# Optimization experiments

Hardware: AMD Instinct MI355X
Metric: run time of the kernel (lower is better)

Reference implementation:

```python
import jax, jax.numpy as jnp
import numpy as np

B, P, D, H = 4, 2048, 768, 12
DFF = 4 * D
EPS = 1e-3  # Keras LayerNormalization default epsilon
SURVIVAL_PROB = 0.9  # inference-mode droppath scaling


def setup_inputs() -> dict:
    key = jax.random.key(0)
    ks = jax.random.split(key, 4)
    s = 0.02
    return {
        "x": jax.random.normal(ks[0], (B, P, D), dtype=jnp.float32),
        "ln1_g": jnp.ones((D,), jnp.float32),
        "ln1_b": jnp.zeros((D,), jnp.float32),
        "w_qkv": jax.random.normal(ks[1], (D, 3 * D), jnp.float32) * s,
        "b_qkv": jnp.zeros((3 * D,), jnp.float32),
        "ln2_g": jnp.ones((D,), jnp.float32),
        "ln2_b": jnp.zeros((D,), jnp.float32),
        "w1": jax.random.normal(ks[2], (D, DFF), jnp.float32) * s,
        "b1": jnp.zeros((DFF,), jnp.float32),
        "w2": jax.random.normal(ks[3], (DFF, D), jnp.float32) * s,
        "b2": jnp.zeros((D,), jnp.float32),
    }


def _layernorm(x, g, b):
    mu = jnp.mean(x, axis=-1, keepdims=True)
    var = jnp.mean(jnp.square(x - mu), axis=-1, keepdims=True)
    return (x - mu) * jax.lax.rsqrt(var + EPS) * g + b


def _block(x, ln1_g, ln1_b, w_qkv, b_qkv, ln2_g, ln2_b, w1, b1, w2, b2):
    # --- pre-norm self-attention ---
    h = _layernorm(x, ln1_g, ln1_b)
    qkv = h @ w_qkv + b_qkv                      # [B,P,3D]
    q, k, v = jnp.split(qkv, 3, axis=-1)
    hd = D // H
    to_heads = lambda t: t.reshape(B, P, H, hd).transpose(0, 2, 1, 3)  # b h p c
    q, k, v = to_heads(q), to_heads(k), to_heads(v)
    scale = jnp.sqrt(jnp.float32(D / H))
    scores = jnp.einsum('bhqc,bhkc->bhqk', q, k) / scale
    attn = jax.nn.softmax(scores, axis=-1)
    o = jnp.einsum('bhqk,bhkc->bhqc', attn, v)
    o = o.transpose(0, 2, 1, 3).reshape(B, P, D)
    x = o * SURVIVAL_PROB + x
    # --- pre-norm MLP ---
    h = _layernorm(x, ln2_g, ln2_b)
    h = jax.nn.gelu(h @ w1 + b1, approximate=False)
    h = h @ w2 + b2
    return h * SURVIVAL_PROB + x


def reference(x, ln1_g, ln1_b, w_qkv, b_qkv, ln2_g, ln2_b, w1, b1, w2, b2):
    return _block(x, ln1_g, ln1_b, w_qkv, b_qkv, ln2_g, ln2_b, w1, b1, w2, b2)
```

## Files before the change

kernel.cpp:

```cpp
#include <hip/hip_runtime.h>
#include <hip/hip_bf16.h>
#include <math.h>

#define B_ 4
#define P_ 2048
#define D_ 768
#define H_ 12

typedef __attribute__((ext_vector_type(8))) short bf16x8;
typedef __attribute__((ext_vector_type(4))) float f32x4;

static __device__ __forceinline__ short f2bf(float f) {
  union { float f; unsigned u; } z; z.f = f;
  unsigned r = z.u + 0x7fffu + ((z.u >> 16) & 1u);
  return (short)(r >> 16);
}

static __device__ __forceinline__ void gll16(const void* g, void* l) {
  __builtin_amdgcn_global_load_lds(
      (const __attribute__((address_space(1))) void*)g,
      (__attribute__((address_space(3))) void*)l, 16, 0, 0);
}

static __device__ __forceinline__ int vswz(int d) {
  return ((d & 7) ^ ((d >> 3) & 7)) << 3;
}

__global__ __launch_bounds__(256) void tcvt_kernel(const float* __restrict__ in,
                                                   short* __restrict__ out, int K, int N) {
  __shared__ float t[32][33];
  int k0 = blockIdx.x * 32, n0 = blockIdx.y * 32;
  int tx = threadIdx.x & 31, ty = threadIdx.x >> 5;
#pragma unroll
  for (int i = 0; i < 4; ++i)
    t[ty + 8 * i][tx] = in[(size_t)(k0 + ty + 8 * i) * N + n0 + tx];
  __syncthreads();
#pragma unroll
  for (int i = 0; i < 4; ++i)
    out[(size_t)(n0 + ty + 8 * i) * K + k0 + tx] = f2bf(t[tx][ty + 8 * i]);
}

__global__ __launch_bounds__(256) void ln_kernel(const float* __restrict__ in,
                                                 const float* __restrict__ g,
                                                 const float* __restrict__ be,
                                                 short* __restrict__ out) {
  int row = blockIdx.x, tid = threadIdx.x;
  const float* xr = in + (size_t)row * D_;
  float v0 = xr[tid], v1 = xr[tid + 256], v2 = xr[tid + 512];
  float s = v0 + v1 + v2;
  float ss = v0 * v0 + v1 * v1 + v2 * v2;
#pragma unroll
  for (int d = 1; d < 64; d <<= 1) {
    s += __shfl_xor(s, d, 64);
    ss += __shfl_xor(ss, d, 64);
  }
  __shared__ float red[8];
  int w = tid >> 6;
  if ((tid & 63) == 0) { red[w] = s; red[4 + w] = ss; }
  __syncthreads();
  s = red[0] + red[1] + red[2] + red[3];
  ss = red[4] + red[5] + red[6] + red[7];
  float mu = s * (1.0f / D_);
  float rstd = rsqrtf(ss * (1.0f / D_) - mu * mu + 1e-3f);
  short* orow = out + (size_t)row * D_;
  orow[tid]       = f2bf((v0 - mu) * rstd * g[tid]       + be[tid]);
  orow[tid + 256] = f2bf((v1 - mu) * rstd * g[tid + 256] + be[tid + 256]);
  orow[tid + 512] = f2bf((v2 - mu) * rstd * g[tid + 512] + be[tid + 512]);
}

template <int EPI>
__global__ __launch_bounds__(256, 3) void gemm128(
    const short* __restrict__ A, const short* __restrict__ Bt,
    const float* __restrict__ bias, short* __restrict__ out_bf,
    float* __restrict__ out_f, const float* __restrict__ resid,
    int M, int N, int K) {
  alignas(16) __shared__ short a_lds[128 * 32];
  alignas(16) __shared__ short b_lds[128 * 32];
  const int tid = threadIdx.x;
  const int wv = tid >> 6, lane = tid & 63;
  const int wm = wv >> 1, wn = wv & 1;
  const int g = lane >> 4, r = lane & 15;
  const int m0 = blockIdx.x * 128, n0 = blockIdx.y * 128;
  const int srow = lane >> 2, sseg = lane & 3;
  f32x4 acc[4][4] = {};
  const short* aptr = A + (size_t)(m0 + wv * 16 + srow) * K + sseg * 8;
  const short* bptr = Bt + (size_t)(n0 + wv * 16 + srow) * K + sseg * 8;
  short* alds0 = &a_lds[(wv * 16) * 32];
  short* blds0 = &b_lds[(wv * 16) * 32];
  for (int k0 = 0; k0 < K; k0 += 32) {
    __syncthreads();
    gll16(aptr + k0, alds0);
    gll16(aptr + k0 + (size_t)64 * K, alds0 + 64 * 32);
    gll16(bptr + k0, blds0);
    gll16(bptr + k0 + (size_t)64 * K, blds0 + 64 * 32);
    __syncthreads();
    bf16x8 af[4], bfr[4];
#pragma unroll
    for (int i = 0; i < 4; ++i)
      af[i] = *reinterpret_cast<const bf16x8*>(&a_lds[(wm * 64 + i * 16 + r) * 32 + g * 8]);
#pragma unroll
    for (int i = 0; i < 4; ++i)
      bfr[i] = *reinterpret_cast<const bf16x8*>(&b_lds[(wn * 64 + i * 16 + r) * 32 + g * 8]);
#pragma unroll
    for (int i = 0; i < 4; ++i)
#pragma unroll
      for (int jn = 0; jn < 4; ++jn)
        acc[i][jn] = __builtin_amdgcn_mfma_f32_16x16x32_bf16(af[i], bfr[jn], acc[i][jn], 0, 0, 0);
  }
#pragma unroll
  for (int i = 0; i < 4; ++i) {
#pragma unroll
    for (int jn = 0; jn < 4; ++jn) {
      int col = n0 + wn * 64 + jn * 16 + r;
      float bb = bias[col];
#pragma unroll
      for (int jj = 0; jj < 4; ++jj) {
        int row = m0 + wm * 64 + i * 16 + g * 4 + jj;
        float v = acc[i][jn][jj] + bb;
        size_t idx = (size_t)row * N + col;
        if (EPI == 0) {
          out_bf[idx] = f2bf(v);
        } else if (EPI == 1) {
          v = 0.5f * v * (1.0f + erff(v * 0.70710678118654752f));
          out_bf[idx] = f2bf(v);
        } else {
          out_f[idx] = v * 0.9f + resid[idx];
        }
      }
    }
  }
}

__global__ __launch_bounds__(256, 3) void attn_kernel(const short* __restrict__ qkv,
                                                      const float* __restrict__ x,
                                                      float* __restrict__ x2) {
  alignas(16) __shared__ short k_lds[64 * 72];
  alignas(16) __shared__ short vt_lds[64 * 64];
  alignas(16) __shared__ short p_lds[4][32 * 72];
  const int tid = threadIdx.x, wv = tid >> 6, lane = tid & 63;
  const int g = lane >> 4, r = lane & 15;
  const int b = blockIdx.y / H_, h = blockIdx.y % H_;
  const int TD = 3 * D_;
  const int qrow0 = blockIdx.x * 128 + wv * 32;
  bf16x8 qf[2][2];
#pragma unroll
  for (int mf = 0; mf < 2; ++mf)
#pragma unroll
    for (int kb = 0; kb < 2; ++kb)
      qf[mf][kb] = *reinterpret_cast<const bf16x8*>(
          qkv + (size_t)(b * P_ + qrow0 + mf * 16 + r) * TD + h * 64 + kb * 32 + g * 8);
  f32x4 acc[2][4] = {};
  float m_run[2][4], l_run[2][4];
#pragma unroll
  for (int mf = 0; mf < 2; ++mf)
#pragma unroll
    for (int j = 0; j < 4; ++j) { m_run[mf][j] = -1e30f; l_run[mf][j] = 0.0f; }
  const int lrow = tid >> 2, lseg = tid & 3;
  short* p_w = &p_lds[wv][0];
  for (int kc = 0; kc < P_; kc += 64) {
    const short* src = qkv + (size_t)(b * P_ + kc + lrow) * TD + D_ + h * 64 + lseg * 16;
    bf16x8 kv0 = *reinterpret_cast<const bf16x8*>(src);
    bf16x8 kv1 = *reinterpret_cast<const bf16x8*>(src + 8);
    bf16x8 vv0 = *reinterpret_cast<const bf16x8*>(src + D_);
    bf16x8 vv1 = *reinterpret_cast<const bf16x8*>(src + D_ + 8);
    __syncthreads();
    *reinterpret_cast<bf16x8*>(&k_lds[lrow * 72 + lseg * 16]) = kv0;
    *reinterpret_cast<bf16x8*>(&k_lds[lrow * 72 + lseg * 16 + 8]) = kv1;
#pragma unroll
    for (int j = 0; j < 8; ++j) {
      int d0 = lseg * 16 + j, d1 = d0 + 8;
      vt_lds[d0 * 64 + (lrow ^ vswz(d0))] = vv0[j];
      vt_lds[d1 * 64 + (lrow ^ vswz(d1))] = vv1[j];
    }
    __syncthreads();
    f32x4 sc[2][4];
#pragma unroll
    for (int cf = 0; cf < 4; ++cf) {
      bf16x8 kf0 = *reinterpret_cast<const bf16x8*>(&k_lds[(cf * 16 + r) * 72 + g * 8]);
      bf16x8 kf1 = *reinterpret_cast<const bf16x8*>(&k_lds[(cf * 16 + r) * 72 + 32 + g * 8]);
#pragma unroll
      for (int mf = 0; mf < 2; ++mf) {
        f32x4 s = {};
        s = __builtin_amdgcn_mfma_f32_16x16x32_bf16(qf[mf][0], kf0, s, 0, 0, 0);
        s = __builtin_amdgcn_mfma_f32_16x16x32_bf16(qf[mf][1], kf1, s, 0, 0, 0);
        sc[mf][cf] = s;
      }
    }
#pragma unroll
    for (int mf = 0; mf < 2; ++mf) {
#pragma unroll
      for (int j = 0; j < 4; ++j) {
        float s0 = sc[mf][0][j] * 0.125f, s1 = sc[mf][1][j] * 0.125f;
        float s2 = sc[mf][2][j] * 0.125f, s3 = sc[mf][3][j] * 0.125f;
        float mt = fmaxf(fmaxf(s0, s1), fmaxf(s2, s3));
#pragma unroll
        for (int d = 1; d < 16; d <<= 1) mt = fmaxf(mt, __shfl_xor(mt, d, 64));
        float mn = fmaxf(m_run[mf][j], mt);
        float corr = __expf(m_run[mf][j] - mn);
        m_run[mf][j] = mn;
        float p0 = __expf(s0 - mn), p1 = __expf(s1 - mn);
        float p2 = __expf(s2 - mn), p3 = __expf(s3 - mn);
        float ls = p0 + p1 + p2 + p3;
#pragma unroll
        for (int d = 1; d < 16; d <<= 1) ls += __shfl_xor(ls, d, 64);
        l_run[mf][j] = l_run[mf][j] * corr + ls;
#pragma unroll
        for (int cf = 0; cf < 4; ++cf) acc[mf][cf][j] *= corr;
        int prow = (mf * 16 + g * 4 + j) * 72;
        p_w[prow + 0 + r]  = f2bf(p0);
        p_w[prow + 16 + r] = f2bf(p1);
        p_w[prow + 32 + r] = f2bf(p2);
        p_w[prow + 48 + r] = f2bf(p3);
      }
    }
    bf16x8 vf[4][2];
#pragma unroll
    for (int cf = 0; cf < 4; ++cf) {
      int d = cf * 16 + r;
      int sw = vswz(d);
      vf[cf][0] = *reinterpret_cast<const bf16x8*>(&vt_lds[d * 64 + ((g * 8) ^ sw)]);
      vf[cf][1] = *reinterpret_cast<const bf16x8*>(&vt_lds[d * 64 + ((32 + g * 8) ^ sw)]);
    }
#pragma unroll
    for (int mf = 0; mf < 2; ++mf) {
      bf16x8 pf0 = *reinterpret_cast<const bf16x8*>(&p_w[(mf * 16 + r) * 72 + g * 8]);
      bf16x8 pf1 = *reinterpret_cast<const bf16x8*>(&p_w[(mf * 16 + r) * 72 + 32 + g * 8]);
#pragma unroll
      for (int cf = 0; cf < 4; ++cf) {
        acc[mf][cf] = __builtin_amdgcn_mfma_f32_16x16x32_bf16(pf0, vf[cf][0], acc[mf][cf], 0, 0, 0);
        acc[mf][cf] = __builtin_amdgcn_mfma_f32_16x16x32_bf16(pf1, vf[cf][1], acc[mf][cf], 0, 0, 0);
      }
    }
  }
#pragma unroll
  for (int mf = 0; mf < 2; ++mf)
#pragma unroll
    for (int cf = 0; cf < 4; ++cf) {
      int col = h * 64 + cf * 16 + r;
#pragma unroll
      for (int j = 0; j < 4; ++j) {
        int row = qrow0 + mf * 16 + g * 4 + j;
        size_t idx = (size_t)(b * P_ + row) * D_ + col;
        x2[idx] = (acc[mf][cf][j] / l_run[mf][j]) * 0.9f + x[idx];
      }
    }
}

extern "C" void kernel_launch(void* const* d_in, const int* in_sizes, int n_in,
                              void* d_out, int out_size, void* d_ws, size_t ws_size,
                              hipStream_t stream) {
  const float* x     = (const float*)d_in[0];
  const float* ln1_g = (const float*)d_in[1];
  const float* ln1_b = (const float*)d_in[2];
  const float* w_qkv = (const float*)d_in[3];
  const float* b_qkv = (const float*)d_in[4];
  const float* ln2_g = (const float*)d_in[5];
  const float* ln2_b = (const float*)d_in[6];
  const float* w1    = (const float*)d_in[7];
  const float* b1    = (const float*)d_in[8];
  const float* w2    = (const float*)d_in[9];
  const float* b2    = (const float*)d_in[10];
  float* out = (float*)d_out;
  char* ws = (char*)d_ws;

  short* wqkv_t = (short*)(ws);
  short* w1_t   = (short*)(ws + 3538944);
  short* w2_t   = (short*)(ws + 8257536);
  short* h_bf   = (short*)(ws + 12976128);
  short* qkv_bf = (short*)(ws + 25559040);
  short* a1_bf  = qkv_bf;

  const int R = B_ * P_;

  { dim3 g2(768 / 32, 2304 / 32);  tcvt_kernel<<<g2, 256, 0, stream>>>(w_qkv, wqkv_t, 768, 2304); }
  { dim3 g2(768 / 32, 3072 / 32);  tcvt_kernel<<<g2, 256, 0, stream>>>(w1, w1_t, 768, 3072); }
  { dim3 g2(3072 / 32, 768 / 32);  tcvt_kernel<<<g2, 256, 0, stream>>>(w2, w2_t, 3072, 768); }

  ln_kernel<<<R, 256, 0, stream>>>(x, ln1_g, ln1_b, h_bf);

  {
    dim3 grid(R / 128, 2304 / 128);
    gemm128<0><<<grid, 256, 0, stream>>>(h_bf, wqkv_t, b_qkv, qkv_bf, nullptr, nullptr,
                                         R, 2304, 768);
  }
  {
    dim3 grid(P_ / 128, B_ * H_);
    attn_kernel<<<grid, 256, 0, stream>>>(qkv_bf, x, out);
  }
  ln_kernel<<<R, 256, 0, stream>>>(out, ln2_g, ln2_b, h_bf);
  {
    dim3 grid(R / 128, 3072 / 128);
    gemm128<1><<<grid, 256, 0, stream>>>(h_bf, w1_t, b1, a1_bf, nullptr, nullptr,
                                         R, 3072, 768);
  }
  {
    dim3 grid(R / 128, 768 / 128);
    gemm128<2><<<grid, 256, 0, stream>>>(a1_bf, w2_t, b2, nullptr, out, out,
                                         R, 768, 3072);
  }
}
```

Before: 460.7 us.

## Compute transposed attention scores so softmax reductions stay mostly in-lane

Swaps the MFMA operands so each lane holds scores for one query row across several keys. The row max and sum then need only two cross-lane shuffles instead of four per row-slot, and P is written to LDS with packed bf16 stores. The 1/8 scale is folded into Q once, with bf16 rounding, and the final normalisation uses a reciprocal broadcast by shuffle. The per-row correction factor now needs extra shuffles to reach the accumulator layout, and pre-scaling Q in bf16 slightly changes rounding.

```diff
diff --git a/kernel.cpp b/kernel.cpp
--- a/kernel.cpp
+++ b/kernel.cpp
@@ -14,6 +14,12 @@
   union { float f; unsigned u; } z; z.f = f;
   unsigned r = z.u + 0x7fffu + ((z.u >> 16) & 1u);
   return (short)(r >> 16);
+}
+
+static __device__ __forceinline__ float bf2f(short s) {
+  union { unsigned u; float f; } z;
+  z.u = ((unsigned)(unsigned short)s) << 16;
+  return z.f;
 }
 
 static __device__ __forceinline__ void gll16(const void* g, void* l) {
@@ -146,17 +152,20 @@
 #pragma unroll
   for (int mf = 0; mf < 2; ++mf)
 #pragma unroll
-    for (int kb = 0; kb < 2; ++kb)
-      qf[mf][kb] = *reinterpret_cast<const bf16x8*>(
+    for (int kb = 0; kb < 2; ++kb) {
+      bf16x8 q = *reinterpret_cast<const bf16x8*>(
           qkv + (size_t)(b * P_ + qrow0 + mf * 16 + r) * TD + h * 64 + kb * 32 + g * 8);
+#pragma unroll
+      for (int e = 0; e < 8; ++e) q[e] = f2bf(bf2f(q[e]) * 0.125f);
+      qf[mf][kb] = q;
+    }
   f32x4 acc[2][4] = {};
-  float m_run[2][4], l_run[2][4];
-#pragma unroll
-  for (int mf = 0; mf < 2; ++mf)
-#pragma unroll
-    for (int j = 0; j < 4; ++j) { m_run[mf][j] = -1e30f; l_run[mf][j] = 0.0f; }
+  float m_run[2], l_run[2];
+#pragma unroll
+  for (int mf = 0; mf < 2; ++mf) { m_run[mf] = -1e30f; l_run[mf] = 0.0f; }
   const int lrow = tid >> 2, lseg = tid & 3;
   short* p_w = &p_lds[wv][0];
+  const int bcast = 20 * g;
   for (int kc = 0; kc < P_; kc += 64) {
     const short* src = qkv + (size_t)(b * P_ + kc + lrow) * TD + D_ + h * 64 + lseg * 16;
     bf16x8 kv0 = *reinterpret_cast<const bf16x8*>(src);
@@ -173,7 +182,7 @@
       vt_lds[d1 * 64 + (lrow ^ vswz(d1))] = vv1[j];
     }
     __syncthreads();
-    f32x4 sc[2][4];
+    f32x4 st[2][4];
 #pragma unroll
     for (int cf = 0; cf < 4; ++cf) {
       bf16x8 kf0 = *reinterpret_cast<const bf16x8*>(&k_lds[(cf * 16 + r) * 72 + g * 8]);
@@ -181,36 +190,53 @@
 #pragma unroll
       for (int mf = 0; mf < 2; ++mf) {
         f32x4 s = {};
-        s = __builtin_amdgcn_mfma_f32_16x16x32_bf16(qf[mf][0], kf0, s, 0, 0, 0);
-        s = __builtin_amdgcn_mfma_f32_16x16x32_bf16(qf[mf][1], kf1, s, 0, 0, 0);
-        sc[mf][cf] = s;
+        s = __builtin_amdgcn_mfma_f32_16x16x32_bf16(kf0, qf[mf][0], s, 0, 0, 0);
+        s = __builtin_amdgcn_mfma_f32_16x16x32_bf16(kf1, qf[mf][1], s, 0, 0, 0);
+        st[mf][cf] = s;
       }
     }
 #pragma unroll
     for (int mf = 0; mf < 2; ++mf) {
-#pragma unroll
-      for (int j = 0; j < 4; ++j) {
-        float s0 = sc[mf][0][j] * 0.125f, s1 = sc[mf][1][j] * 0.125f;
-        float s2 = sc[mf][2][j] * 0.125f, s3 = sc[mf][3][j] * 0.125f;
-        float mt = fmaxf(fmaxf(s0, s1), fmaxf(s2, s3));
-#pragma unroll
-        for (int d = 1; d < 16; d <<= 1) mt = fmaxf(mt, __shfl_xor(mt, d, 64));
-        float mn = fmaxf(m_run[mf][j], mt);
-        float corr = __expf(m_run[mf][j] - mn);
-        m_run[mf][j] = mn;
-        float p0 = __expf(s0 - mn), p1 = __expf(s1 - mn);
-        float p2 = __expf(s2 - mn), p3 = __expf(s3 - mn);
-        float ls = p0 + p1 + p2 + p3;
-#pragma unroll
-        for (int d = 1; d < 16; d <<= 1) ls += __shfl_xor(ls, d, 64);
-        l_run[mf][j] = l_run[mf][j] * corr + ls;
-#pragma unroll
-        for (int cf = 0; cf < 4; ++cf) acc[mf][cf][j] *= corr;
-        int prow = (mf * 16 + g * 4 + j) * 72;
-        p_w[prow + 0 + r]  = f2bf(p0);
-        p_w[prow + 16 + r] = f2bf(p1);
-        p_w[prow + 32 + r] = f2bf(p2);
-        p_w[prow + 48 + r] = f2bf(p3);
+      float mx = st[mf][0][0];
+#pragma unroll
+      for (int cf = 0; cf < 4; ++cf)
+#pragma unroll
+        for (int j = 0; j < 4; ++j) mx = fmaxf(mx, st[mf][cf][j]);
+      mx = fmaxf(mx, __shfl_xor(mx, 16, 64));
+      mx = fmaxf(mx, __shfl_xor(mx, 32, 64));
+      float mn = fmaxf(m_run[mf], mx);
+      float corr = __expf(m_run[mf] - mn);
+      m_run[mf] = mn;
+      float p[4][4];
+      float ls = 0.0f;
+#pragma unroll
+      for (int cf = 0; cf < 4; ++cf)
+#pragma unroll
+        for (int j = 0; j < 4; ++j) {
+          float pv = __expf(st[mf][cf][j] - mn);
+          p[cf][j] = pv;
+          ls += pv;
+        }
+      ls += __shfl_xor(ls, 16, 64);
+      ls += __shfl_xor(ls, 32, 64);
+      l_run[mf] = l_run[mf] * corr + ls;
+      short* prow = &p_w[(mf * 16 + r) * 72];
+#pragma unroll
+      for (int cf = 0; cf < 4; ++cf) {
+        __hip_bfloat162 lo = __float22bfloat162_rn(make_float2(p[cf][0], p[cf][1]));
+        __hip_bfloat162 hi = __float22bfloat162_rn(make_float2(p[cf][2], p[cf][3]));
+        union { __hip_bfloat162 h2; unsigned u; } c0, c1;
+        c0.h2 = lo; c1.h2 = hi;
+        *reinterpret_cast<uint2*>(&prow[cf * 16 + 4 * g]) = make_uint2(c0.u, c1.u);
+      }
+      float cb0 = __shfl(corr, bcast + 0, 64);
+      float cb1 = __shfl(corr, bcast + 1, 64);
+      float cb2 = __shfl(corr, bcast + 2, 64);
+      float cb3 = __shfl(corr, bcast + 3, 64);
+#pragma unroll
+      for (int cf = 0; cf < 4; ++cf) {
+        acc[mf][cf][0] *= cb0; acc[mf][cf][1] *= cb1;
+        acc[mf][cf][2] *= cb2; acc[mf][cf][3] *= cb3;
       }
     }
     bf16x8 vf[4][2];
@@ -233,7 +259,12 @@
     }
   }
 #pragma unroll
-  for (int mf = 0; mf < 2; ++mf)
+  for (int mf = 0; mf < 2; ++mf) {
+    float lb0 = 0.9f / __shfl(l_run[mf], bcast + 0, 64);
+    float lb1 = 0.9f / __shfl(l_run[mf], bcast + 1, 64);
+    float lb2 = 0.9f / __shfl(l_run[mf], bcast + 2, 64);
+    float lb3 = 0.9f / __shfl(l_run[mf], bcast + 3, 64);
+    float lb[4] = {lb0, lb1, lb2, lb3};
 #pragma unroll
     for (int cf = 0; cf < 4; ++cf) {
       int col = h * 64 + cf * 16 + r;
@@ -241,9 +272,10 @@
       for (int j = 0; j < 4; ++j) {
         int row = qrow0 + mf * 16 + g * 4 + j;
         size_t idx = (size_t)(b * P_ + row) * D_ + col;
-        x2[idx] = (acc[mf][cf][j] / l_run[mf][j]) * 0.9f + x[idx];
-      }
-    }
+        x2[idx] = acc[mf][cf][j] * lb[j] + x[idx];
+      }
+    }
+  }
 }
 
 extern "C" void kernel_launch(void* const* d_in, const int* in_sizes, int n_in,
```

After: 397.3 us. 1.16x faster.
